# Kernel tuning notes

Hardware: AMD Instinct MI355X
Metric: run time of the kernel (lower is better)

## Reference

```python
import jax, jax.numpy as jnp
import numpy as np

D_MODEL = 1024
NHEAD = 16
HEAD_DIM = D_MODEL // NHEAD


def setup_inputs() -> dict:
    key = jax.random.key(0)
    ks = jax.random.split(key, 11)
    B, S, D = 4, 2048, D_MODEL
    scale = 1.0 / np.sqrt(D)
    inp = {
        'q': jax.random.normal(ks[0], (B, S, D), jnp.float32),
        'k': jax.random.normal(ks[1], (B, S, D), jnp.float32),
        'v': jax.random.normal(ks[2], (B, S, D), jnp.float32),
        'Wq': jax.random.normal(ks[3], (D, D), jnp.float32) * scale,
        'bq': jnp.zeros((D,), jnp.float32),
        'Wk': jax.random.normal(ks[4], (D, D), jnp.float32) * scale,
        'bk': jnp.zeros((D,), jnp.float32),
        'Wv': jax.random.normal(ks[5], (D, D), jnp.float32) * scale,
        'bv': jnp.zeros((D,), jnp.float32),
        'Wo': jax.random.normal(ks[6], (D, D), jnp.float32) * scale,
        'bo': jnp.zeros((D,), jnp.float32),
    }
    return inp


def reference(q, k, v, Wq, bq, Wk, bk, Wv, bv, Wo, bo):
    B, S, D = q.shape
    H, Hd = NHEAD, HEAD_DIM
    # projections (torch Linear: x @ W.T + b), then split heads -> [B,H,S,Hd]
    qh = (q @ Wq.T + bq).reshape(B, S, H, Hd).transpose(0, 2, 1, 3)
    kh = (k @ Wk.T + bk).reshape(B, S, H, Hd).transpose(0, 2, 1, 3)
    vh = (v @ Wv.T + bv).reshape(B, S, H, Hd).transpose(0, 2, 1, 3)
    # scaled dot-product attention (mask=None, dropout eval-mode identity)
    scores = jnp.einsum('bhqd,bhkd->bhqk', qh, kh) / jnp.sqrt(jnp.float32(Hd))
    attn = jax.nn.softmax(scores, axis=-1)
    out = jnp.einsum('bhqk,bhkd->bhqd', attn, vh)  # [B,H,S,Hd]
    out = out.transpose(0, 2, 1, 3).reshape(B, S, D)
    return out @ Wo.T + bo
```

## Files before the change

kernel.cpp:

```cpp
#include <hip/hip_runtime.h>
#include <cstdint>

using u16 = unsigned short;
using u32 = unsigned int;
typedef __bf16 bf16x8 __attribute__((ext_vector_type(8)));
typedef float f32x4 __attribute__((ext_vector_type(4)));
typedef float f32x16 __attribute__((ext_vector_type(16)));
typedef u16 u16x8 __attribute__((ext_vector_type(8)));
typedef u16 u16x4 __attribute__((ext_vector_type(4)));

#define DEV static __device__ __forceinline__

DEV u16 f2bf(float f) {
  uint32_t u = __builtin_bit_cast(uint32_t, f);
  u += 0x7FFFu + ((u >> 16) & 1u);
  return (u16)(u >> 16);
}
DEV float bf2f(u16 h) {
  uint32_t u = ((uint32_t)h) << 16;
  return __builtin_bit_cast(float, u);
}
DEV u32 cvt_pk_bf16(float lo, float hi) {
  u32 r;
  asm("v_cvt_pk_bf16_f32 %0, %1, %2" : "=v"(r) : "v"(lo), "v"(hi));
  return r;
}

typedef const u32 __attribute__((address_space(1))) gcu32;
typedef u32 __attribute__((address_space(3))) lu32;
DEV void gl_lds16(const u16* g, u16* l) {
  __builtin_amdgcn_global_load_lds((gcu32*)g, (lu32*)l, 16, 0, 0);
}

#define MFMA(a, b, c) __builtin_amdgcn_mfma_f32_16x16x32_bf16((a), (b), (c), 0, 0, 0)
#define MFMA32(a, b, c) __builtin_amdgcn_mfma_f32_32x32x16_bf16((a), (b), (c), 0, 0, 0)

__global__ __launch_bounds__(256) void cvt_all(
    const float* __restrict__ q, const float* __restrict__ k,
    const float* __restrict__ v, const float* __restrict__ Wq,
    const float* __restrict__ Wk, const float* __restrict__ Wv,
    const float* __restrict__ Wo, u16* __restrict__ Xb, u16* __restrict__ Wb,
    u16* __restrict__ WoB) {
  const int bid = blockIdx.x;
  const float* src;
  u16* dst;
  size_t i;
  if (bid < 12288) {
    const int z = bid >> 12;
    src = (z == 0) ? q : (z == 1) ? k : v;
    dst = Xb + (size_t)z * 8388608;
    i = ((size_t)(bid & 4095) * 256 + threadIdx.x) * 8;
  } else {
    const int r = bid - 12288;
    const int z = r >> 9;
    src = (z == 0) ? Wq : (z == 1) ? Wk : (z == 2) ? Wv : Wo;
    dst = (z < 3) ? (Wb + (size_t)z * 1048576) : WoB;
    i = ((size_t)(r & 511) * 256 + threadIdx.x) * 8;
  }
  const float4 a = *(const float4*)(src + i);
  const float4 b = *(const float4*)(src + i + 4);
  u16x8 o;
  o[0] = f2bf(a.x); o[1] = f2bf(a.y); o[2] = f2bf(a.z); o[3] = f2bf(a.w);
  o[4] = f2bf(b.x); o[5] = f2bf(b.y); o[6] = f2bf(b.z); o[7] = f2bf(b.w);
  *(u16x8*)(dst + i) = o;
}

__global__ __launch_bounds__(256) void proj_gemm_bf(
    const u16* __restrict__ Xb, const u16* __restrict__ Wb,
    const float* __restrict__ bq, const float* __restrict__ bk,
    const float* __restrict__ bv, u16* __restrict__ Qh, u16* __restrict__ Kh,
    u16* __restrict__ Vt) {
  __shared__ u16 As[2][128 * 64];
  __shared__ u16 Bs[2][128 * 64];
  const int z = blockIdx.z;
  const int m0 = blockIdx.y * 128, n0 = blockIdx.x * 128;

  const u16* x = Xb + (size_t)z * 8388608;
  const u16* W = Wb + (size_t)z * 1048576;
  const float* bias = (z == 0) ? bq : (z == 1) ? bk : bv;
  u16* out = (z == 0) ? Qh : (z == 1) ? Kh : Vt;
  const float oscale = (z == 0) ? 0.18033688011112042f : 1.0f;

  const int tid = threadIdx.x;
  const int w = tid >> 6, lane = tid & 63;
  const int wr = w >> 1, wc = w & 1;
  const int lr = lane & 15, lk = (lane >> 4) * 8;
  const int hq = lane >> 4;

  const int srow = w * 8 + (lane >> 3);
  const int scol = ((lane & 7) ^ ((lane >> 3) & 7)) * 8;
  const u16* xg = x + (size_t)(m0 + srow) * 1024 + scol;
  const u16* wg_ = W + (size_t)(n0 + srow) * 1024 + scol;

  f32x4 acc[4][4];
  const f32x4 fzero = {0.f, 0.f, 0.f, 0.f};
#pragma unroll
  for (int m = 0; m < 4; ++m)
#pragma unroll
    for (int n = 0; n < 4; ++n) acc[m][n] = fzero;

#define PROJ_STAGE(buf, k0)                                                  \
  {                                                                          \
    _Pragma("unroll") for (int c = 0; c < 4; ++c) {                          \
      gl_lds16(xg + (size_t)c * 32 * 1024 + (k0), &As[buf][c * 2048 + w * 512]); \
      gl_lds16(wg_ + (size_t)c * 32 * 1024 + (k0), &Bs[buf][c * 2048 + w * 512]); \
    }                                                                        \
  }

  PROJ_STAGE(0, 0);
  asm volatile("s_waitcnt vmcnt(0)" ::: "memory");
  __syncthreads();

  int cur = 0;
  for (int kt = 0; kt < 16; ++kt) {
    if (kt < 15) PROJ_STAGE(cur ^ 1, (kt + 1) * 64);
#pragma unroll
    for (int kk = 0; kk < 2; ++kk) {
      bf16x8 a[4], b[4];
#pragma unroll
      for (int m = 0; m < 4; ++m) {
        const int row = wr * 64 + m * 16 + lr;
        a[m] = *(const bf16x8*)&As[cur][row * 64 + (((kk * 4 + hq) ^ (lr & 7)) * 8)];
      }
#pragma unroll
      for (int n = 0; n < 4; ++n) {
        const int row = wc * 64 + n * 16 + lr;
        b[n] = *(const bf16x8*)&Bs[cur][row * 64 + (((kk * 4 + hq) ^ (lr & 7)) * 8)];
      }
#pragma unroll
      for (int m = 0; m < 4; ++m)
#pragma unroll
        for (int n = 0; n < 4; ++n) acc[m][n] = MFMA(a[m], b[n], acc[m][n]);
    }
    asm volatile("s_waitcnt vmcnt(0)" ::: "memory");
    __syncthreads();
    cur ^= 1;
  }
#undef PROJ_STAGE

#pragma unroll
  for (int n = 0; n < 4; ++n) {
    const int col = n0 + wc * 64 + n * 16 + lr;
    const float bvv = bias[col];
    const int h = col >> 6, d = col & 63;
#pragma unroll
    for (int m = 0; m < 4; ++m) {
#pragma unroll
      for (int j = 0; j < 4; ++j) {
        const int rowg = m0 + wr * 64 + m * 16 + (lane >> 4) * 4 + j;
        const int bb = rowg >> 11, s = rowg & 2047;
        const float val = (acc[m][n][j] + bvv) * oscale;
        size_t idx;
        if (z != 2)
          idx = ((size_t)(bb * 16 + h) * 2048 + s) * 64 + d;
        else
          idx = ((size_t)(bb * 16 + h) * 64 + d) * 2048 + s;
        out[idx] = f2bf(val);
      }
    }
  }
}

__global__ __launch_bounds__(256) void proj_gemm_f32(
    const float* __restrict__ q, const float* __restrict__ k,
    const float* __restrict__ v, const float* __restrict__ Wq,
    const float* __restrict__ Wk, const float* __restrict__ Wv,
    const float* __restrict__ bq, const float* __restrict__ bk,
    const float* __restrict__ bv, u16* __restrict__ Qh, u16* __restrict__ Kh,
    u16* __restrict__ Vt) {
  __shared__ u16 As[128][40];
  __shared__ u16 Bs[128][40];
  const int z = blockIdx.z;
  const float* x = (z == 0) ? q : (z == 1) ? k : v;
  const float* W = (z == 0) ? Wq : (z == 1) ? Wk : Wv;
  const float* bias = (z == 0) ? bq : (z == 1) ? bk : bv;
  u16* out = (z == 0) ? Qh : (z == 1) ? Kh : Vt;
  const float oscale = (z == 0) ? 0.18033688011112042f : 1.0f;

  const int tid = threadIdx.x;
  const int m0 = blockIdx.y * 128, n0 = blockIdx.x * 128;
  const int w = tid >> 6, lane = tid & 63;
  const int wr = w >> 1, wc = w & 1;
  const int lr = lane & 15, lk = (lane >> 4) * 8;
  const int srow = tid >> 3, sc4 = (tid & 7) * 4;

  f32x4 acc[4][4];
  const f32x4 fzero = {0.f, 0.f, 0.f, 0.f};
#pragma unroll
  for (int m = 0; m < 4; ++m)
#pragma unroll
    for (int n = 0; n < 4; ++n) acc[m][n] = fzero;

  for (int kt = 0; kt < 32; ++kt) {
    const int k0 = kt * 32;
    __syncthreads();
#pragma unroll
    for (int c = 0; c < 4; ++c) {
      const float4 av = *(const float4*)(x + (size_t)(m0 + c * 32 + srow) * 1024 + k0 + sc4);
      const float4 bvv = *(const float4*)(W + (size_t)(n0 + c * 32 + srow) * 1024 + k0 + sc4);
      u16x4 ah, bh;
      ah[0] = f2bf(av.x); ah[1] = f2bf(av.y); ah[2] = f2bf(av.z); ah[3] = f2bf(av.w);
      bh[0] = f2bf(bvv.x); bh[1] = f2bf(bvv.y); bh[2] = f2bf(bvv.z); bh[3] = f2bf(bvv.w);
      *(u16x4*)&As[c * 32 + srow][sc4] = ah;
      *(u16x4*)&Bs[c * 32 + srow][sc4] = bh;
    }
    __syncthreads();
    bf16x8 a[4], b[4];
#pragma unroll
    for (int m = 0; m < 4; ++m)
      a[m] = *(const bf16x8*)&As[wr * 64 + m * 16 + lr][lk];
#pragma unroll
    for (int n = 0; n < 4; ++n)
      b[n] = *(const bf16x8*)&Bs[wc * 64 + n * 16 + lr][lk];
#pragma unroll
    for (int m = 0; m < 4; ++m)
#pragma unroll
      for (int n = 0; n < 4; ++n) acc[m][n] = MFMA(a[m], b[n], acc[m][n]);
  }

#pragma unroll
  for (int n = 0; n < 4; ++n) {
    const int col = n0 + wc * 64 + n * 16 + lr;
    const float bvv = bias[col];
    const int h = col >> 6, d = col & 63;
#pragma unroll
    for (int m = 0; m < 4; ++m) {
#pragma unroll
      for (int j = 0; j < 4; ++j) {
        const int rowg = m0 + wr * 64 + m * 16 + (lane >> 4) * 4 + j;
        const int bb = rowg >> 11, s = rowg & 2047;
        const float val = (acc[m][n][j] + bvv) * oscale;
        size_t idx;
        if (z != 2)
          idx = ((size_t)(bb * 16 + h) * 2048 + s) * 64 + d;
        else
          idx = ((size_t)(bb * 16 + h) * 64 + d) * 2048 + s;
        out[idx] = f2bf(val);
      }
    }
  }
}

__global__ __launch_bounds__(512, 4) void attn_fwd(
    const u16* __restrict__ Qh, const u16* __restrict__ Kh,
    const u16* __restrict__ Vt, u16* __restrict__ Att) {
  __shared__ u16 Ks[64][72];
  __shared__ u16 Vs[64][72];
  const int tid = threadIdx.x;
  const int w = tid >> 6, lane = tid & 63;
  const int lq = lane & 31, h = lane >> 5;
  const int head = blockIdx.x, q0 = blockIdx.y * 256;
  const u16* Qb = Qh + (size_t)head * 131072;
  const u16* Kb = Kh + (size_t)head * 131072;
  const u16* Vb = Vt + (size_t)head * 131072;
  const int qrow = q0 + w * 32 + lq;

  bf16x8 qf[4];
#pragma unroll
  for (int dc = 0; dc < 4; ++dc)
    qf[dc] = *(const bf16x8*)(Qb + (size_t)qrow * 64 + dc * 16 + h * 8);

  u16x8 ou;
#pragma unroll
  for (int j = 0; j < 8; ++j) ou[j] = 0x3F80;
  const bf16x8 ones = __builtin_bit_cast(bf16x8, ou);

  f32x16 o0 = {}, o1 = {}, osum = {};

  const int srow = tid >> 3, scol = (tid & 7) * 8;
  uint4 kr, vr;
  kr = *(const uint4*)(Kb + (size_t)srow * 64 + scol);
  vr = *(const uint4*)(Vb + (size_t)srow * 2048 + scol);

  for (int kt = 0; kt < 32; ++kt) {
    __syncthreads();
    *(uint4*)&Ks[srow][scol] = kr;
    *(uint4*)&Vs[srow][scol] = vr;
    __syncthreads();
    if (kt + 1 < 32) {
      const int t0n = (kt + 1) * 64;
      kr = *(const uint4*)(Kb + (size_t)(t0n + srow) * 64 + scol);
      vr = *(const uint4*)(Vb + (size_t)srow * 2048 + t0n + scol);
    }

    f32x16 s0 = {}, s1 = {};
    __builtin_amdgcn_s_setprio(1);
#pragma unroll
    for (int dc = 0; dc < 4; ++dc) {
      const bf16x8 k0 = *(const bf16x8*)&Ks[lq][dc * 16 + h * 8];
      const bf16x8 k1 = *(const bf16x8*)&Ks[32 + lq][dc * 16 + h * 8];
      s0 = MFMA32(k0, qf[dc], s0);
      s1 = MFMA32(k1, qf[dc], s1);
    }
    __builtin_amdgcn_s_setprio(0);

#pragma unroll
    for (int r = 0; r < 16; ++r) {
      s0[r] = __builtin_amdgcn_exp2f(s0[r]);
      s1[r] = __builtin_amdgcn_exp2f(s1[r]);
    }

    u32 w0[8], w1[8];
#pragma unroll
    for (int b = 0; b < 4; ++b)
#pragma unroll
      for (int e = 0; e < 2; ++e) {
        w0[b * 2 + e] = cvt_pk_bf16(s0[4 * b + 2 * e], s0[4 * b + 2 * e + 1]);
        w1[b * 2 + e] = cvt_pk_bf16(s1[4 * b + 2 * e], s1[4 * b + 2 * e + 1]);
      }

    bf16x8 pa[4];
#pragma unroll
    for (int c = 0; c < 2; ++c) {
      u32 a0 = w0[(2 * c) * 2 + 0], b0 = w0[(2 * c + 1) * 2 + 0];
      u32 a1 = w0[(2 * c) * 2 + 1], b1 = w0[(2 * c + 1) * 2 + 1];
      asm("v_permlane32_swap_b32 %0, %1" : "+v"(a0), "+v"(b0));
      asm("v_permlane32_swap_b32 %0, %1" : "+v"(a1), "+v"(b1));
      const uint4 f = {a0, a1, b0, b1};
      pa[c] = __builtin_bit_cast(bf16x8, f);
    }
#pragma unroll
    for (int c = 0; c < 2; ++c) {
      u32 a0 = w1[(2 * c) * 2 + 0], b0 = w1[(2 * c + 1) * 2 + 0];
      u32 a1 = w1[(2 * c) * 2 + 1], b1 = w1[(2 * c + 1) * 2 + 1];
      asm("v_permlane32_swap_b32 %0, %1" : "+v"(a0), "+v"(b0));
      asm("v_permlane32_swap_b32 %0, %1" : "+v"(a1), "+v"(b1));
      const uint4 f = {a0, a1, b0, b1};
      pa[2 + c] = __builtin_bit_cast(bf16x8, f);
    }

    __builtin_amdgcn_s_setprio(1);
#pragma unroll
    for (int c = 0; c < 4; ++c) {
      const bf16x8 v0f = *(const bf16x8*)&Vs[lq][c * 16 + h * 8];
      const bf16x8 v1f = *(const bf16x8*)&Vs[32 + lq][c * 16 + h * 8];
      o0 = MFMA32(pa[c], v0f, o0);
      o1 = MFMA32(pa[c], v1f, o1);
      osum = MFMA32(pa[c], ones, osum);
    }
    __builtin_amdgcn_s_setprio(0);
  }

  const int bb = head >> 4, hh = head & 15;
#pragma unroll
  for (int r = 0; r < 16; ++r) {
    const int qr = (r & 3) + 8 * (r >> 2) + 4 * h;
    const float li = 1.0f / osum[r];
    const int qg = q0 + w * 32 + qr;
    const size_t base = ((size_t)(bb * 2048 + qg)) * 1024 + hh * 64;
    Att[base + lq] = f2bf(o0[r] * li);
    Att[base + 32 + lq] = f2bf(o1[r] * li);
  }
}

__global__ __launch_bounds__(256) void out_gemm_bf(
    const u16* __restrict__ Att, const u16* __restrict__ WoB,
    const float* __restrict__ bo, float* __restrict__ out) {
  __shared__ u16 As[2][128 * 64];
  __shared__ u16 Bs[2][128 * 64];
  const int m0 = blockIdx.y * 128, n0 = blockIdx.x * 128;
  const int tid = threadIdx.x;
  const int w = tid >> 6, lane = tid & 63;
  const int wr = w >> 1, wc = w & 1;
  const int lr = lane & 15;
  const int hq = lane >> 4;

  const int srow = w * 8 + (lane >> 3);
  const int scol = ((lane & 7) ^ ((lane >> 3) & 7)) * 8;
  const u16* ag = Att + (size_t)(m0 + srow) * 1024 + scol;
  const u16* bg = WoB + (size_t)(n0 + srow) * 1024 + scol;

  f32x4 acc[4][4];
  const f32x4 fzero = {0.f, 0.f, 0.f, 0.f};
#pragma unroll
  for (int m = 0; m < 4; ++m)
#pragma unroll
    for (int n = 0; n < 4; ++n) acc[m][n] = fzero;

#define OUT_STAGE(buf, k0)                                                   \
  {                                                                          \
    _Pragma("unroll") for (int c = 0; c < 4; ++c) {                          \
      gl_lds16(ag + (size_t)c * 32 * 1024 + (k0), &As[buf][c * 2048 + w * 512]); \
      gl_lds16(bg + (size_t)c * 32 * 1024 + (k0), &Bs[buf][c * 2048 + w * 512]); \
    }                                                                        \
  }

  OUT_STAGE(0, 0);
  asm volatile("s_waitcnt vmcnt(0)" ::: "memory");
  __syncthreads();

  int cur = 0;
  for (int kt = 0; kt < 16; ++kt) {
    if (kt < 15) OUT_STAGE(cur ^ 1, (kt + 1) * 64);
#pragma unroll
    for (int kk = 0; kk < 2; ++kk) {
      bf16x8 a[4], b[4];
#pragma unroll
      for (int m = 0; m < 4; ++m) {
        const int row = wr * 64 + m * 16 + lr;
        a[m] = *(const bf16x8*)&As[cur][row * 64 + (((kk * 4 + hq) ^ (lr & 7)) * 8)];
      }
#pragma unroll
      for (int n = 0; n < 4; ++n) {
        const int row = wc * 64 + n * 16 + lr;
        b[n] = *(const bf16x8*)&Bs[cur][row * 64 + (((kk * 4 + hq) ^ (lr & 7)) * 8)];
      }
#pragma unroll
      for (int m = 0; m < 4; ++m)
#pragma unroll
        for (int n = 0; n < 4; ++n) acc[m][n] = MFMA(a[m], b[n], acc[m][n]);
    }
    asm volatile("s_waitcnt vmcnt(0)" ::: "memory");
    __syncthreads();
    cur ^= 1;
  }
#undef OUT_STAGE

#pragma unroll
  for (int n = 0; n < 4; ++n) {
    const int col = n0 + wc * 64 + n * 16 + lr;
    const float bvv = bo[col];
#pragma unroll
    for (int m = 0; m < 4; ++m)
#pragma unroll
      for (int j = 0; j < 4; ++j) {
        const int rowg = m0 + wr * 64 + m * 16 + (lane >> 4) * 4 + j;
        out[(size_t)rowg * 1024 + col] = acc[m][n][j] + bvv;
      }
  }
}

__global__ __launch_bounds__(256) void out_gemm_f32(
    const u16* __restrict__ Att, const float* __restrict__ Wo,
    const float* __restrict__ bo, float* __restrict__ out) {
  __shared__ u16 As[128][40], Bs[128][40];
  const int tid = threadIdx.x;
  const int m0 = blockIdx.y * 128, n0 = blockIdx.x * 128;
  const int w = tid >> 6, lane = tid & 63;
  const int wr = w >> 1, wc = w & 1;
  const int lr = lane & 15, lk = (lane >> 4) * 8;
  const int arow = tid >> 2, ac8 = (tid & 3) * 8;
  const int wrow = tid >> 3, wc4 = (tid & 7) * 4;

  f32x4 acc[4][4];
  const f32x4 fzero = {0.f, 0.f, 0.f, 0.f};
#pragma unroll
  for (int m = 0; m < 4; ++m)
#pragma unroll
    for (int n = 0; n < 4; ++n) acc[m][n] = fzero;

  for (int kt = 0; kt < 32; ++kt) {
    const int k0 = kt * 32;
    __syncthreads();
#pragma unroll
    for (int c = 0; c < 2; ++c) {
      *(uint4*)&As[c * 64 + arow][ac8] =
          *(const uint4*)(Att + (size_t)(m0 + c * 64 + arow) * 1024 + k0 + ac8);
    }
#pragma unroll
    for (int c = 0; c < 4; ++c) {
      const float4 wv = *(const float4*)(Wo + (size_t)(n0 + c * 32 + wrow) * 1024 + k0 + wc4);
      u16x4 hv;
      hv[0] = f2bf(wv.x); hv[1] = f2bf(wv.y); hv[2] = f2bf(wv.z); hv[3] = f2bf(wv.w);
      *(u16x4*)&Bs[c * 32 + wrow][wc4] = hv;
    }
    __syncthreads();
    bf16x8 a[4], b[4];
#pragma unroll
    for (int m = 0; m < 4; ++m)
      a[m] = *(const bf16x8*)&As[wr * 64 + m * 16 + lr][lk];
#pragma unroll
    for (int n = 0; n < 4; ++n)
      b[n] = *(const bf16x8*)&Bs[wc * 64 + n * 16 + lr][lk];
#pragma unroll
    for (int m = 0; m < 4; ++m)
#pragma unroll
      for (int n = 0; n < 4; ++n) acc[m][n] = MFMA(a[m], b[n], acc[m][n]);
  }

#pragma unroll
  for (int n = 0; n < 4; ++n) {
    const int col = n0 + wc * 64 + n * 16 + lr;
    const float bvv = bo[col];
#pragma unroll
    for (int m = 0; m < 4; ++m)
#pragma unroll
      for (int j = 0; j < 4; ++j) {
        const int rowg = m0 + wr * 64 + m * 16 + (lane >> 4) * 4 + j;
        out[(size_t)rowg * 1024 + col] = acc[m][n][j] + bvv;
      }
  }
}

extern "C" void kernel_launch(void* const* d_in, const int* in_sizes, int n_in,
                              void* d_out, int out_size, void* d_ws, size_t ws_size,
                              hipStream_t stream) {
  const float* q  = (const float*)d_in[0];
  const float* k  = (const float*)d_in[1];
  const float* v  = (const float*)d_in[2];
  const float* Wq = (const float*)d_in[3];
  const float* bq = (const float*)d_in[4];
  const float* Wk = (const float*)d_in[5];
  const float* bk = (const float*)d_in[6];
  const float* Wv = (const float*)d_in[7];
  const float* bv = (const float*)d_in[8];
  const float* Wo = (const float*)d_in[9];
  const float* bo = (const float*)d_in[10];

  u16* ws  = (u16*)d_ws;
  u16* Qh  = ws;
  u16* Kh  = ws + (size_t)8388608;
  u16* Vt  = ws + (size_t)16777216;
  u16* Att = ws + (size_t)25165824;
  u16* Xb  = ws + (size_t)25165824;
  u16* Wb  = ws + (size_t)50331648;
  u16* WoB = ws + (size_t)53477376;
  const size_t need = (size_t)55574528 * 2;

  if (ws_size >= need) {
    cvt_all<<<dim3(14336), dim3(256), 0, stream>>>(q, k, v, Wq, Wk, Wv, Wo, Xb,
                                                   Wb, WoB);
    proj_gemm_bf<<<dim3(8, 64, 3), dim3(256), 0, stream>>>(Xb, Wb, bq, bk, bv,
                                                           Qh, Kh, Vt);
    attn_fwd<<<dim3(64, 8), dim3(512), 0, stream>>>(Qh, Kh, Vt, Att);
    out_gemm_bf<<<dim3(8, 64), dim3(256), 0, stream>>>(Att, WoB, bo,
                                                       (float*)d_out);
  } else {
    proj_gemm_f32<<<dim3(8, 64, 3), dim3(256), 0, stream>>>(
        q, k, v, Wq, Wk, Wv, bq, bk, bv, Qh, Kh, Vt);
    attn_fwd<<<dim3(64, 8), dim3(512), 0, stream>>>(Qh, Kh, Vt, Att);
    out_gemm_f32<<<dim3(8, 64), dim3(256), 0, stream>>>(Att, Wo, bo,
                                                        (float*)d_out);
  }
}
```

Measured before the change: 237.5 us.

## Pipeline GEMM loads with partial vmcnt waits, priority hints, and swapped grid order

In the bf16 projection and output GEMMs, the K loop is now fully unrolled. Each step prefetches the next stage and waits only on the older loads (vmcnt(8)) instead of draining every load, so more memory traffic can overlap with the MFMAs. The MFMA section is wrapped in s_setprio and sched_barrier, with raw s_barrier placed at both ends. The grid is transposed so consecutive blocks walk along M for a fixed N tile, which changes which weight and activation tiles share L2.

```diff
diff --git a/kernel.cpp b/kernel.cpp
--- a/kernel.cpp
+++ b/kernel.cpp
@@ -34,6 +34,8 @@
 
 #define MFMA(a, b, c) __builtin_amdgcn_mfma_f32_16x16x32_bf16((a), (b), (c), 0, 0, 0)
 #define MFMA32(a, b, c) __builtin_amdgcn_mfma_f32_32x32x16_bf16((a), (b), (c), 0, 0, 0)
+
+#define WAITV(n) asm volatile("s_waitcnt vmcnt(" #n ")" ::: "memory")
 
 __global__ __launch_bounds__(256) void cvt_all(
     const float* __restrict__ q, const float* __restrict__ k,
@@ -73,7 +75,7 @@
   __shared__ u16 As[2][128 * 64];
   __shared__ u16 Bs[2][128 * 64];
   const int z = blockIdx.z;
-  const int m0 = blockIdx.y * 128, n0 = blockIdx.x * 128;
+  const int m0 = blockIdx.x * 128, n0 = blockIdx.y * 128;
 
   const u16* x = Xb + (size_t)z * 8388608;
   const u16* W = Wb + (size_t)z * 1048576;
@@ -84,8 +86,7 @@
   const int tid = threadIdx.x;
   const int w = tid >> 6, lane = tid & 63;
   const int wr = w >> 1, wc = w & 1;
-  const int lr = lane & 15, lk = (lane >> 4) * 8;
-  const int hq = lane >> 4;
+  const int lr = lane & 15, hq = lane >> 4;
 
   const int srow = w * 8 + (lane >> 3);
   const int scol = ((lane & 7) ^ ((lane >> 3) & 7)) * 8;
@@ -99,21 +100,30 @@
 #pragma unroll
     for (int n = 0; n < 4; ++n) acc[m][n] = fzero;
 
-#define PROJ_STAGE(buf, k0)                                                  \
-  {                                                                          \
-    _Pragma("unroll") for (int c = 0; c < 4; ++c) {                          \
-      gl_lds16(xg + (size_t)c * 32 * 1024 + (k0), &As[buf][c * 2048 + w * 512]); \
-      gl_lds16(wg_ + (size_t)c * 32 * 1024 + (k0), &Bs[buf][c * 2048 + w * 512]); \
-    }                                                                        \
-  }
-
-  PROJ_STAGE(0, 0);
-  asm volatile("s_waitcnt vmcnt(0)" ::: "memory");
-  __syncthreads();
-
-  int cur = 0;
-  for (int kt = 0; kt < 16; ++kt) {
-    if (kt < 15) PROJ_STAGE(cur ^ 1, (kt + 1) * 64);
+#define PSTAGE(b, t)                                                          \
+  {                                                                           \
+    _Pragma("unroll") for (int c = 0; c < 4; ++c) {                           \
+      gl_lds16(xg + (size_t)c * 32 * 1024 + (t) * 64,                         \
+               &As[b][c * 2048 + w * 512]);                                   \
+      gl_lds16(wg_ + (size_t)c * 32 * 1024 + (t) * 64,                        \
+               &Bs[b][c * 2048 + w * 512]);                                   \
+    }                                                                         \
+  }
+
+  PSTAGE(0, 0);
+
+#pragma unroll
+  for (int t = 0; t < 16; ++t) {
+    const int cur = t & 1;
+    if (t < 15) {
+      PSTAGE(cur ^ 1, t + 1);
+      WAITV(8);
+    } else {
+      WAITV(0);
+    }
+    __builtin_amdgcn_s_barrier();
+    __builtin_amdgcn_sched_barrier(0);
+    __builtin_amdgcn_s_setprio(1);
 #pragma unroll
     for (int kk = 0; kk < 2; ++kk) {
       bf16x8 a[4], b[4];
@@ -132,11 +142,11 @@
 #pragma unroll
         for (int n = 0; n < 4; ++n) acc[m][n] = MFMA(a[m], b[n], acc[m][n]);
     }
-    asm volatile("s_waitcnt vmcnt(0)" ::: "memory");
-    __syncthreads();
-    cur ^= 1;
-  }
-#undef PROJ_STAGE
+    __builtin_amdgcn_s_setprio(0);
+    __builtin_amdgcn_sched_barrier(0);
+    __builtin_amdgcn_s_barrier();
+  }
+#undef PSTAGE
 
 #pragma unroll
   for (int n = 0; n < 4; ++n) {
@@ -147,7 +157,7 @@
     for (int m = 0; m < 4; ++m) {
 #pragma unroll
       for (int j = 0; j < 4; ++j) {
-        const int rowg = m0 + wr * 64 + m * 16 + (lane >> 4) * 4 + j;
+        const int rowg = m0 + wr * 64 + m * 16 + hq * 4 + j;
         const int bb = rowg >> 11, s = rowg & 2047;
         const float val = (acc[m][n][j] + bvv) * oscale;
         size_t idx;
@@ -358,12 +368,11 @@
     const float* __restrict__ bo, float* __restrict__ out) {
   __shared__ u16 As[2][128 * 64];
   __shared__ u16 Bs[2][128 * 64];
-  const int m0 = blockIdx.y * 128, n0 = blockIdx.x * 128;
+  const int m0 = blockIdx.x * 128, n0 = blockIdx.y * 128;
   const int tid = threadIdx.x;
   const int w = tid >> 6, lane = tid & 63;
   const int wr = w >> 1, wc = w & 1;
-  const int lr = lane & 15;
-  const int hq = lane >> 4;
+  const int lr = lane & 15, hq = lane >> 4;
 
   const int srow = w * 8 + (lane >> 3);
   const int scol = ((lane & 7) ^ ((lane >> 3) & 7)) * 8;
@@ -377,21 +386,30 @@
 #pragma unroll
     for (int n = 0; n < 4; ++n) acc[m][n] = fzero;
 
-#define OUT_STAGE(buf, k0)                                                   \
-  {                                                                          \
-    _Pragma("unroll") for (int c = 0; c < 4; ++c) {                          \
-      gl_lds16(ag + (size_t)c * 32 * 1024 + (k0), &As[buf][c * 2048 + w * 512]); \
-      gl_lds16(bg + (size_t)c * 32 * 1024 + (k0), &Bs[buf][c * 2048 + w * 512]); \
-    }                                                                        \
-  }
-
-  OUT_STAGE(0, 0);
-  asm volatile("s_waitcnt vmcnt(0)" ::: "memory");
-  __syncthreads();
-
-  int cur = 0;
-  for (int kt = 0; kt < 16; ++kt) {
-    if (kt < 15) OUT_STAGE(cur ^ 1, (kt + 1) * 64);
+#define OSTAGE(b, t)                                                          \
+  {                                                                           \
+    _Pragma("unroll") for (int c = 0; c < 4; ++c) {                           \
+      gl_lds16(ag + (size_t)c * 32 * 1024 + (t) * 64,                         \
+               &As[b][c * 2048 + w * 512]);                                   \
+      gl_lds16(bg + (size_t)c * 32 * 1024 + (t) * 64,                         \
+               &Bs[b][c * 2048 + w * 512]);                                   \
+    }                                                                         \
+  }
+
+  OSTAGE(0, 0);
+
+#pragma unroll
+  for (int t = 0; t < 16; ++t) {
+    const int cur = t & 1;
+    if (t < 15) {
+      OSTAGE(cur ^ 1, t + 1);
+      WAITV(8);
+    } else {
+      WAITV(0);
+    }
+    __builtin_amdgcn_s_barrier();
+    __builtin_amdgcn_sched_barrier(0);
+    __builtin_amdgcn_s_setprio(1);
 #pragma unroll
     for (int kk = 0; kk < 2; ++kk) {
       bf16x8 a[4], b[4];
@@ -410,11 +428,11 @@
 #pragma unroll
         for (int n = 0; n < 4; ++n) acc[m][n] = MFMA(a[m], b[n], acc[m][n]);
     }
-    asm volatile("s_waitcnt vmcnt(0)" ::: "memory");
-    __syncthreads();
-    cur ^= 1;
-  }
-#undef OUT_STAGE
+    __builtin_amdgcn_s_setprio(0);
+    __builtin_amdgcn_sched_barrier(0);
+    __builtin_amdgcn_s_barrier();
+  }
+#undef OSTAGE
 
 #pragma unroll
   for (int n = 0; n < 4; ++n) {
@@ -424,7 +442,7 @@
     for (int m = 0; m < 4; ++m)
 #pragma unroll
       for (int j = 0; j < 4; ++j) {
-        const int rowg = m0 + wr * 64 + m * 16 + (lane >> 4) * 4 + j;
+        const int rowg = m0 + wr * 64 + m * 16 + hq * 4 + j;
         out[(size_t)rowg * 1024 + col] = acc[m][n][j] + bvv;
       }
   }
@@ -520,10 +538,10 @@
   if (ws_size >= need) {
     cvt_all<<<dim3(14336), dim3(256), 0, stream>>>(q, k, v, Wq, Wk, Wv, Wo, Xb,
                                                    Wb, WoB);
-    proj_gemm_bf<<<dim3(8, 64, 3), dim3(256), 0, stream>>>(Xb, Wb, bq, bk, bv,
+    proj_gemm_bf<<<dim3(64, 8, 3), dim3(256), 0, stream>>>(Xb, Wb, bq, bk, bv,
                                                            Qh, Kh, Vt);
     attn_fwd<<<dim3(64, 8), dim3(512), 0, stream>>>(Qh, Kh, Vt, Att);
-    out_gemm_bf<<<dim3(8, 64), dim3(256), 0, stream>>>(Att, WoB, bo,
+    out_gemm_bf<<<dim3(64, 8), dim3(256), 0, stream>>>(Att, WoB, bo,
                                                        (float*)d_out);
   } else {
     proj_gemm_f32<<<dim3(8, 64, 3), dim3(256), 0, stream>>>(
```

After: 193.7 us. 18.4% less time.
